# Performance work log

Hardware: AMD Instinct MI355X
Metric: run time of the kernel (lower is better)

## Reference

```python
import jax, jax.numpy as jnp
import numpy as np

N = 100_000   # nodes
E = 1_600_000 # edges
V = 100_000   # vocab
G = 256       # graphs in batch
D = 64        # emb/hidden dim


def setup_inputs() -> dict:
    key = jax.random.key(0)
    ks = jax.random.split(key, 12)
    x_tokens = jax.random.randint(ks[0], (N, 1), 0, V)
    edge_index = jax.random.randint(ks[1], (2, E), 0, N)
    batch = jnp.sort(jax.random.randint(ks[2], (N,), 0, G))
    s = 0.02
    return {
        "x_tokens": x_tokens,
        "edge_index": edge_index,
        "batch": batch,
        "emb_table": jax.random.normal(ks[3], (V, D), jnp.float32) * s,
        "W0": jax.random.normal(ks[4], (D, D), jnp.float32) * s,
        "b0": jnp.zeros((D,), jnp.float32),
        "W1": jax.random.normal(ks[5], (D, D), jnp.float32) * s,
        "b1": jnp.zeros((D,), jnp.float32),
        "W2": jax.random.normal(ks[6], (D, D), jnp.float32) * s,
        "b2": jnp.zeros((D,), jnp.float32),
        "Wc1": jax.random.normal(ks[7], (2 * D, D), jnp.float32) * s,
        "bc1": jnp.zeros((D,), jnp.float32),
        "Wc2": jax.random.normal(ks[8], (D, 2), jnp.float32) * s,
        "bc2": jnp.zeros((2,), jnp.float32),
    }


def _gcn_norm(edge_index, n_nodes):
    # add self loops, compute symmetric normalization coefficients
    loop = jnp.arange(n_nodes, dtype=edge_index.dtype)
    src = jnp.concatenate([edge_index[0], loop])
    dst = jnp.concatenate([edge_index[1], loop])
    deg = jax.ops.segment_sum(jnp.ones_like(dst, jnp.float32), dst, num_segments=n_nodes)
    dinv = jnp.where(deg > 0, deg ** -0.5, 0.0)
    norm = dinv[src] * dinv[dst]  # [E+N]
    return src, dst, norm


def _gcn_conv(x, W, b, src, dst, norm, n_nodes):
    x = x @ W                                   # [N, D]
    msg = x[src] * norm[:, None]                # gather + scale, [E+N, D]
    out = jax.ops.segment_sum(msg, dst, num_segments=n_nodes)
    return out + b


def reference(x_tokens, edge_index, batch, emb_table, W0, b0, W1, b1, W2, b2, Wc1, bc1, Wc2, bc2):
    n = x_tokens.shape[0]
    src, dst, norm = _gcn_norm(edge_index, n)
    x = emb_table[x_tokens[:, 0]]               # [N, D]
    for W, b in ((W0, b0), (W1, b1), (W2, b2)):
        x = jax.nn.relu(_gcn_conv(x, W, b, src, dst, norm, n))
    # dual pooling over graph ids
    cnt = jax.ops.segment_sum(jnp.ones((n,), x.dtype), batch, num_segments=G)
    h_sum = jax.ops.segment_sum(x, batch, num_segments=G)
    h_mean = h_sum / jnp.maximum(cnt, 1.0)[:, None]
    h_max = jax.ops.segment_max(x, batch, num_segments=G)
    h_max = jnp.where(jnp.isfinite(h_max), h_max, 0.0)
    h = jnp.concatenate([h_mean, h_max], axis=-1)   # [G, 2D]
    logits = jax.nn.relu(h @ Wc1 + bc1) @ Wc2 + bc2  # [G, 2]
    return logits
```

## Files before the change

kernel.cpp:

```cpp
#include <hip/hip_runtime.h>
#include <hip/hip_fp16.h>
#include <math.h>


#define BKT_LOG 9
#define BKT (1 << BKT_LOG)
#define CHUNK 4096

typedef _Float16 h2 __attribute__((ext_vector_type(2)));
typedef _Float16 f16x8 __attribute__((ext_vector_type(8)));
typedef float f32x4 __attribute__((ext_vector_type(4)));

__global__ __launch_bounds__(256) void k_wcvt(const float* __restrict__ W0,
                                              const float* __restrict__ W1,
                                              const float* __restrict__ W2,
                                              _Float16* __restrict__ Wf,
                                              int* __restrict__ gcur,
                                              float* __restrict__ hz, int hzn) {
  if (blockIdx.x < 3) {
    const float* W = (blockIdx.x == 0) ? W0 : (blockIdx.x == 1) ? W1 : W2;
    _Float16* out = Wf + blockIdx.x * 4096;
    for (int i = threadIdx.x; i < 4096; i += 256) {
      int c = i >> 10, s = (i >> 9) & 1, l = (i >> 3) & 63, j = i & 7;
      int k = 32 * s + 8 * (l >> 4) + j;
      int ncol = 16 * c + (l & 15);
      out[i] = (_Float16)W[k * 64 + ncol];
    }
  } else if (blockIdx.x == 3) {
    gcur[threadIdx.x] = 0;
  } else {
    for (int i = threadIdx.x; i < hzn; i += 256) hz[i] = 0.f;
  }
}

__global__ __launch_bounds__(256) void k_part(const int* __restrict__ src,
                                              const int* __restrict__ dst,
                                              int* __restrict__ gcur,
                                              int* __restrict__ ebuf,
                                              int E, int S) {
  __shared__ int sA[CHUNK];
  __shared__ int dA[CHUNK];
  __shared__ int h[256], base[256];
  int tid = threadIdx.x;
  long c0 = (long)blockIdx.x * CHUNK;
  int m = (int)min((long)CHUNK, (long)E - c0);
  h[tid] = 0;
  __syncthreads();
  for (int i = tid; i < m; i += 256) {
    int s = src[c0 + i];
    int d = dst[c0 + i];
    sA[i] = s;
    dA[i] = d;
    atomicAdd(&h[d >> BKT_LOG], 1);
  }
  __syncthreads();
  if (h[tid]) base[tid] = atomicAdd(&gcur[tid], h[tid]);
  __syncthreads();
  h[tid] = 0;
  __syncthreads();
  for (int i = tid; i < m; i += 256) {
    int s = sA[i], d = dA[i];
    int k = d >> BKT_LOG;
    int p = base[k] + atomicAdd(&h[k], 1);
    if (p < S)
      ebuf[k * S + p] = ((d & (BKT - 1)) << 17) | s;
  }
}

__global__ __launch_bounds__(512) void k_bplace(const int* __restrict__ ebuf,
                                                const int* __restrict__ gcur,
                                                int* __restrict__ off,
                                                int* __restrict__ eend,
                                                int* __restrict__ csrc,
                                                float* __restrict__ dinv,
                                                int N, int S) {
  __shared__ int s[512];
  __shared__ int cur[512];
  int b = blockIdx.x, tid = threadIdx.x;
  int n0 = b << BKT_LOG;
  int nn = min(BKT, N - n0);
  int e0 = b * S;
  int cnt = min(gcur[b], S);
  s[tid] = 0;
  __syncthreads();
  for (int e = tid; e < cnt; e += 512) atomicAdd(&s[ebuf[e0 + e] >> 17], 1);
  __syncthreads();
  int deg = s[tid];
  for (int d = 1; d < 512; d <<= 1) {
    int t = (tid >= d) ? s[tid - d] : 0;
    __syncthreads();
    s[tid] += t;
    __syncthreads();
  }
  int excl = s[tid] - deg;
  if (tid < nn) {
    off[n0 + tid] = e0 + excl;
    eend[n0 + tid] = e0 + excl + deg;
    dinv[n0 + tid] = 1.0f / sqrtf((float)(1 + deg));
  }
  cur[tid] = excl;
  __syncthreads();
  for (int e = tid; e < cnt; e += 512) {
    int p = ebuf[e0 + e];
    int pos = e0 + atomicAdd(&cur[p >> 17], 1);
    csrc[pos] = p & 0x1FFFF;
  }
}

template <bool EMB>
__global__ __launch_bounds__(256) void k_mfmamm(const _Float16* __restrict__ y,
                                                const int* __restrict__ tok,
                                                const float* __restrict__ emb,
                                                const _Float16* __restrict__ Wf,
                                                const float* __restrict__ dinv,
                                                float scale,
                                                _Float16* __restrict__ xh,
                                                int n) {
  __shared__ _Float16 lds[4 * 16 * 72];
  int w = threadIdx.x >> 6, l = threadIdx.x & 63;
  int m = l & 15, q = l >> 4;
  int rbase = blockIdx.x * 64 + w * 16;

  f16x8 a0, a1;
  if (EMB) {
    int node = min(rbase + m, n - 1);
    const float* er = emb + (size_t)tok[node] * 64;
    float4 v0 = *(const float4*)(er + q * 8);
    float4 v1 = *(const float4*)(er + q * 8 + 4);
    float4 v2 = *(const float4*)(er + 32 + q * 8);
    float4 v3 = *(const float4*)(er + 32 + q * 8 + 4);
    a0[0] = (_Float16)v0.x; a0[1] = (_Float16)v0.y; a0[2] = (_Float16)v0.z; a0[3] = (_Float16)v0.w;
    a0[4] = (_Float16)v1.x; a0[5] = (_Float16)v1.y; a0[6] = (_Float16)v1.z; a0[7] = (_Float16)v1.w;
    a1[0] = (_Float16)v2.x; a1[1] = (_Float16)v2.y; a1[2] = (_Float16)v2.z; a1[3] = (_Float16)v2.w;
    a1[4] = (_Float16)v3.x; a1[5] = (_Float16)v3.y; a1[6] = (_Float16)v3.z; a1[7] = (_Float16)v3.w;
  } else {
    int node = rbase + m;
    const _Float16* yr = y + ((size_t)(unsigned)node << 6);
    a0 = *(const f16x8*)(yr + q * 8);
    a1 = *(const f16x8*)(yr + 32 + q * 8);
  }
  float4 d4 = *(const float4*)(dinv + rbase + q * 4);

  const f16x8* wf = (const f16x8*)Wf + l;
  f32x4 acc[4];
#pragma unroll
  for (int c = 0; c < 4; c++) {
    f32x4 z = {0.f, 0.f, 0.f, 0.f};
    z = __builtin_amdgcn_mfma_f32_16x16x32_f16(a0, wf[(c * 2 + 0) * 64], z, 0, 0, 0);
    z = __builtin_amdgcn_mfma_f32_16x16x32_f16(a1, wf[(c * 2 + 1) * 64], z, 0, 0, 0);
    acc[c] = z;
  }

  const float ds[4] = {d4.x * scale, d4.y * scale, d4.z * scale, d4.w * scale};
  _Float16* ldw = lds + w * 16 * 72;
#pragma unroll
  for (int c = 0; c < 4; c++)
#pragma unroll
    for (int r = 0; r < 4; r++)
      ldw[(q * 4 + r) * 72 + c * 16 + m] = (_Float16)(acc[c][r] * ds[r]);
  __syncthreads();

  int row2 = l & 15, c2 = l >> 4;
  int node = rbase + row2;
  if (node < n) {
    const uint4* s4 = (const uint4*)(ldw + row2 * 72 + c2 * 16);
    uint4 v0 = s4[0], v1 = s4[1];
    uint4* dst = (uint4*)(xh + ((size_t)(unsigned)node << 6) + c2 * 16);
    dst[0] = v0;
    dst[1] = v1;
  }
}

__global__ __launch_bounds__(256) void k_aggregate(const int* __restrict__ off,
                                                   const int* __restrict__ eend,
                                                   const int* __restrict__ csrc,
                                                   const float* __restrict__ dinv,
                                                   const _Float16* __restrict__ xh,
                                                   const float* __restrict__ bias,
                                                   _Float16* __restrict__ outp,
                                                   int n) {
  int lane = threadIdx.x & 63;
  int t = __builtin_amdgcn_readfirstlane(blockIdx.x * 4 + (threadIdx.x >> 6));
  if (t >= n) return;
  int e0 = off[t];
  int e1 = eend[t];

  float acc = (float)xh[((size_t)(unsigned)t << 6) + lane];
  int e = e0;
  for (; e + 4 <= e1; e += 4) {
    int s0 = csrc[e];
    int s1 = csrc[e + 1];
    int s2 = csrc[e + 2];
    int s3 = csrc[e + 3];
    float v0 = (float)xh[((size_t)(unsigned)s0 << 6) + lane];
    float v1 = (float)xh[((size_t)(unsigned)s1 << 6) + lane];
    float v2 = (float)xh[((size_t)(unsigned)s2 << 6) + lane];
    float v3 = (float)xh[((size_t)(unsigned)s3 << 6) + lane];
    acc += v0;
    acc += v1;
    acc += v2;
    acc += v3;
  }
  for (; e < e1; ++e)
    acc += (float)xh[((size_t)(unsigned)csrc[e] << 6) + lane];

  float sc = dinv[t] * (1.0f / 256.0f);
  float o = fmaxf(acc * sc + bias[lane], 0.f) * 4096.f;
  outp[((size_t)(unsigned)t << 6) + lane] = (_Float16)o;
}

__global__ __launch_bounds__(256) void k_pool(const _Float16* __restrict__ x,
                                              const int* __restrict__ batch,
                                              float* __restrict__ hsum,
                                              float* __restrict__ hmax,
                                              int* __restrict__ cntg,
                                              int n) {
  int wid = (blockIdx.x * blockDim.x + threadIdx.x) >> 6;
  int lane = threadIdx.x & 63;
  int i0 = wid * 64;
  if (i0 >= n) return;
  int i1 = min(i0 + 64, n);
  int batch_l = (i0 + lane < n) ? batch[i0 + lane] : 0;
  float gsum = 0.f, gmax = 0.f;
  int cur = __shfl(batch_l, 0);
  int c = 0;
  for (int i = i0; i < i1; i++) {
    int g = __shfl(batch_l, i - i0);
    if (g != cur) {
      atomicAdd(&hsum[cur * 64 + lane], gsum);
      atomicMax((int*)&hmax[cur * 64 + lane], __float_as_int(gmax));
      if (lane == 0) atomicAdd(&cntg[cur], c);
      gsum = 0.f; gmax = 0.f; c = 0; cur = g;
    }
    float v = (float)x[((size_t)(unsigned)i << 6) + lane];
    gsum += v;
    gmax = fmaxf(gmax, v);
    c++;
  }
  atomicAdd(&hsum[cur * 64 + lane], gsum);
  atomicMax((int*)&hmax[cur * 64 + lane], __float_as_int(gmax));
  if (lane == 0) atomicAdd(&cntg[cur], c);
}

__global__ __launch_bounds__(64) void k_cls(const float* __restrict__ hsum,
                                            const float* __restrict__ hmax,
                                            const int* __restrict__ cnt,
                                            const float* __restrict__ Wc1,
                                            const float* __restrict__ bc1,
                                            const float* __restrict__ Wc2,
                                            const float* __restrict__ bc2,
                                            float* __restrict__ out) {
  __shared__ float h[128];
  __shared__ float hid[64];
  int g = blockIdx.x, j = threadIdx.x;
  int c = cnt[g];
  float cf = (float)(c > 0 ? c : 1);
  h[j] = hsum[g * 64 + j] / cf * (1.0f / 4096.0f);
  h[64 + j] = hmax[g * 64 + j] * (1.0f / 4096.0f);
  __syncthreads();
  float acc = bc1[j];
  for (int k = 0; k < 128; k++) acc += h[k] * Wc1[k * 64 + j];
  hid[j] = fmaxf(acc, 0.f);
  __syncthreads();
  if (j < 2) {
    float a = bc2[j];
    for (int k = 0; k < 64; k++) a += hid[k] * Wc2[k * 2 + j];
    out[g * 2 + j] = a;
  }
}

extern "C" void kernel_launch(void* const* d_in, const int* in_sizes, int n_in,
                              void* d_out, int out_size, void* d_ws, size_t ws_size,
                              hipStream_t stream) {
  const int N = in_sizes[0];
  const int E = in_sizes[1] / 2;
  const int G = out_size / 2;
  const int B = (N + BKT - 1) >> BKT_LOG;
  const int Npad = (N + 63) & ~63;
  const int S = ((((E + B - 1) / B) * 3 / 2 + 256) + 3) & ~3;

  const int* tok   = (const int*)d_in[0];
  const int* ei    = (const int*)d_in[1];
  const int* batch = (const int*)d_in[2];
  const float* emb = (const float*)d_in[3];
  const float* W0 = (const float*)d_in[4];  const float* b0 = (const float*)d_in[5];
  const float* W1 = (const float*)d_in[6];  const float* b1 = (const float*)d_in[7];
  const float* W2 = (const float*)d_in[8];  const float* b2 = (const float*)d_in[9];
  const float* Wc1 = (const float*)d_in[10]; const float* bc1 = (const float*)d_in[11];
  const float* Wc2 = (const float*)d_in[12]; const float* bc2 = (const float*)d_in[13];
  const int* srcp = ei;
  const int* dstp = ei + E;

  int* off    = (int*)d_ws;
  int* eend   = off + N;
  float* dinv = (float*)(eend + N);
  int* gcur   = (int*)(dinv + Npad);
  _Float16* Wf = (_Float16*)(gcur + 256);
  int* csrc   = (int*)(Wf + 3 * 4096);
  _Float16* xh = (_Float16*)(csrc + (size_t)B * S);
  _Float16* y  = xh + (size_t)Npad * 64;
  int* ebuf   = (int*)y;
  float* hsum = (float*)(y + (size_t)Npad * 64);
  float* hmax = hsum + (size_t)G * 64;
  int*   cntg = (int*)(hmax + (size_t)G * 64);

  auto cdiv = [](long a, long b) { return (int)((a + b - 1) / b); };
  const int aggBlocks = cdiv(N, 4);

  k_wcvt<<<5, 256, 0, stream>>>(W0, W1, W2, Wf, gcur, hsum, G * 129);

  k_part<<<cdiv(E, CHUNK), 256, 0, stream>>>(srcp, dstp, gcur, ebuf, E, S);
  k_bplace<<<B, 512, 0, stream>>>(ebuf, gcur, off, eend, csrc, dinv, N, S);

  k_mfmamm<true><<<cdiv(N, 64), 256, 0, stream>>>(nullptr, tok, emb, Wf, dinv, 256.f, xh, N);
  k_aggregate<<<aggBlocks, 256, 0, stream>>>(off, eend, csrc, dinv, xh, b0, y, N);

  k_mfmamm<false><<<cdiv(N, 64), 256, 0, stream>>>(y, nullptr, nullptr, Wf + 4096, dinv, 1.f / 16.f, xh, N);
  k_aggregate<<<aggBlocks, 256, 0, stream>>>(off, eend, csrc, dinv, xh, b1, y, N);

  k_mfmamm<false><<<cdiv(N, 64), 256, 0, stream>>>(y, nullptr, nullptr, Wf + 8192, dinv, 1.f / 16.f, xh, N);
  k_aggregate<<<aggBlocks, 256, 0, stream>>>(off, eend, csrc, dinv, xh, b2, y, N);

  k_pool<<<cdiv(N, 256), 256, 0, stream>>>(y, batch, hsum, hmax, cntg, N);

  k_cls<<<G, 64, 0, stream>>>(hsum, hmax, cntg, Wc1, bc1, Wc2, bc2, (float*)d_out);
}
```

Measured before the change: 342.5 us.

## Fold self-loop into CSR and gather 4-half chunks per lane in aggregation

The bucket placement kernel now writes each node's self-loop into its CSR neighbour list and folds it into the degree, so aggregation needs no separate self term. The aggregation kernel is restructured: each wavefront splits into 4 groups of 16 lanes, each group loads 8 neighbour indices as int4 vectors and gathers 8-byte chunks of the feature row. Values are accumulated with fdot2 against unit masks, then reduced across groups with shuffles. This aims to cut per-edge index loads and issue wider gathers with more loads in flight, at the cost of masked tail handling, a shuffle reduction, and only a quarter of lanes storing.

```diff
diff --git a/kernel.cpp b/kernel.cpp
--- a/kernel.cpp
+++ b/kernel.cpp
@@ -8,8 +8,31 @@
 #define CHUNK 4096
 
 typedef _Float16 h2 __attribute__((ext_vector_type(2)));
+typedef _Float16 f16x4 __attribute__((ext_vector_type(4)));
 typedef _Float16 f16x8 __attribute__((ext_vector_type(8)));
 typedef float f32x4 __attribute__((ext_vector_type(4)));
+
+union HU { unsigned u; h2 h; };
+__device__ inline h2 h2bits(unsigned u) { HU x; x.u = u; return x.h; }
+
+#if __has_builtin(__builtin_amdgcn_fdot2)
+#define FDOT2(a, b, c) __builtin_amdgcn_fdot2((a), (b), (c), false)
+#else
+__device__ inline float FDOT2(h2 a, h2 b, float c) {
+  return (float)a.x * (float)b.x + (float)a.y * (float)b.y + c;
+}
+#endif
+
+#define MASK_X 0x00003C00u
+#define MASK_Y 0x3C000000u
+
+__device__ inline void acc4c(uint2 v, float& a0, float& a1, float& a2, float& a3) {
+  h2 lo = h2bits(v.x), hi = h2bits(v.y);
+  a0 = FDOT2(lo, h2bits(MASK_X), a0);
+  a1 = FDOT2(lo, h2bits(MASK_Y), a1);
+  a2 = FDOT2(hi, h2bits(MASK_X), a2);
+  a3 = FDOT2(hi, h2bits(MASK_Y), a3);
+}
 
 __global__ __launch_bounds__(256) void k_wcvt(const float* __restrict__ W0,
                                               const float* __restrict__ W1,
@@ -80,25 +103,26 @@
   int n0 = b << BKT_LOG;
   int nn = min(BKT, N - n0);
   int e0 = b * S;
-  int cnt = min(gcur[b], S);
-  s[tid] = 0;
+  int cnt = min(gcur[b], S - nn);
+  s[tid] = (tid < nn) ? 1 : 0;
   __syncthreads();
   for (int e = tid; e < cnt; e += 512) atomicAdd(&s[ebuf[e0 + e] >> 17], 1);
   __syncthreads();
-  int deg = s[tid];
+  int degws = s[tid];
   for (int d = 1; d < 512; d <<= 1) {
     int t = (tid >= d) ? s[tid - d] : 0;
     __syncthreads();
     s[tid] += t;
     __syncthreads();
   }
-  int excl = s[tid] - deg;
+  int excl = s[tid] - degws;
   if (tid < nn) {
     off[n0 + tid] = e0 + excl;
-    eend[n0 + tid] = e0 + excl + deg;
-    dinv[n0 + tid] = 1.0f / sqrtf((float)(1 + deg));
-  }
-  cur[tid] = excl;
+    eend[n0 + tid] = e0 + excl + degws;
+    dinv[n0 + tid] = 1.0f / sqrtf((float)degws);
+    csrc[e0 + excl] = n0 + tid;
+  }
+  cur[tid] = excl + ((tid < nn) ? 1 : 0);
   __syncthreads();
   for (int e = tid; e < cnt; e += 512) {
     int p = ebuf[e0 + e];
@@ -180,33 +204,55 @@
                                                    _Float16* __restrict__ outp,
                                                    int n) {
   int lane = threadIdx.x & 63;
-  int t = __builtin_amdgcn_readfirstlane(blockIdx.x * 4 + (threadIdx.x >> 6));
+  int t = blockIdx.x * 4 + (threadIdx.x >> 6);
   if (t >= n) return;
   int e0 = off[t];
   int e1 = eend[t];
-
-  float acc = (float)xh[((size_t)(unsigned)t << 6) + lane];
-  int e = e0;
-  for (; e + 4 <= e1; e += 4) {
-    int s0 = csrc[e];
-    int s1 = csrc[e + 1];
-    int s2 = csrc[e + 2];
-    int s3 = csrc[e + 3];
-    float v0 = (float)xh[((size_t)(unsigned)s0 << 6) + lane];
-    float v1 = (float)xh[((size_t)(unsigned)s1 << 6) + lane];
-    float v2 = (float)xh[((size_t)(unsigned)s2 << 6) + lane];
-    float v3 = (float)xh[((size_t)(unsigned)s3 << 6) + lane];
-    acc += v0;
-    acc += v1;
-    acc += v2;
-    acc += v3;
-  }
-  for (; e < e1; ++e)
-    acc += (float)xh[((size_t)(unsigned)csrc[e] << 6) + lane];
-
-  float sc = dinv[t] * (1.0f / 256.0f);
-  float o = fmaxf(acc * sc + bias[lane], 0.f) * 4096.f;
-  outp[((size_t)(unsigned)t << 6) + lane] = (_Float16)o;
+  int p = lane >> 4;
+  int f = lane & 15;
+  const char* xb = (const char*)xh;
+
+  float a0 = 0.f, a1 = 0.f, a2 = 0.f, a3 = 0.f;
+  for (int base = (e0 & ~7); base < e1; base += 32) {
+    int my = base + p * 8;
+    int4 iA = {0, 0, 0, 0}, iB = {0, 0, 0, 0};
+    if (my < e1) iA = *(const int4*)(csrc + my);
+    if (my + 4 < e1) iB = *(const int4*)(csrc + my + 4);
+    uint2 v0 = {0,0}, v1 = {0,0}, v2 = {0,0}, v3 = {0,0};
+    uint2 v4 = {0,0}, v5 = {0,0}, v6 = {0,0}, v7 = {0,0};
+    if (my + 0 >= e0 && my + 0 < e1) v0 = *(const uint2*)(xb + ((size_t)(unsigned)iA.x << 7) + f * 8);
+    if (my + 1 >= e0 && my + 1 < e1) v1 = *(const uint2*)(xb + ((size_t)(unsigned)iA.y << 7) + f * 8);
+    if (my + 2 >= e0 && my + 2 < e1) v2 = *(const uint2*)(xb + ((size_t)(unsigned)iA.z << 7) + f * 8);
+    if (my + 3 >= e0 && my + 3 < e1) v3 = *(const uint2*)(xb + ((size_t)(unsigned)iA.w << 7) + f * 8);
+    if (my + 4 >= e0 && my + 4 < e1) v4 = *(const uint2*)(xb + ((size_t)(unsigned)iB.x << 7) + f * 8);
+    if (my + 5 >= e0 && my + 5 < e1) v5 = *(const uint2*)(xb + ((size_t)(unsigned)iB.y << 7) + f * 8);
+    if (my + 6 >= e0 && my + 6 < e1) v6 = *(const uint2*)(xb + ((size_t)(unsigned)iB.z << 7) + f * 8);
+    if (my + 7 >= e0 && my + 7 < e1) v7 = *(const uint2*)(xb + ((size_t)(unsigned)iB.w << 7) + f * 8);
+    acc4c(v0, a0, a1, a2, a3);
+    acc4c(v1, a0, a1, a2, a3);
+    acc4c(v2, a0, a1, a2, a3);
+    acc4c(v3, a0, a1, a2, a3);
+    acc4c(v4, a0, a1, a2, a3);
+    acc4c(v5, a0, a1, a2, a3);
+    acc4c(v6, a0, a1, a2, a3);
+    acc4c(v7, a0, a1, a2, a3);
+  }
+
+  a0 += __shfl_xor(a0, 16); a0 += __shfl_xor(a0, 32);
+  a1 += __shfl_xor(a1, 16); a1 += __shfl_xor(a1, 32);
+  a2 += __shfl_xor(a2, 16); a2 += __shfl_xor(a2, 32);
+  a3 += __shfl_xor(a3, 16); a3 += __shfl_xor(a3, 32);
+
+  if (p == 0) {
+    float sc = dinv[t] * (1.0f / 256.0f);
+    float4 bb = *(const float4*)(bias + f * 4);
+    f16x4 hv;
+    hv[0] = (_Float16)(fmaxf(a0 * sc + bb.x, 0.f) * 4096.f);
+    hv[1] = (_Float16)(fmaxf(a1 * sc + bb.y, 0.f) * 4096.f);
+    hv[2] = (_Float16)(fmaxf(a2 * sc + bb.z, 0.f) * 4096.f);
+    hv[3] = (_Float16)(fmaxf(a3 * sc + bb.w, 0.f) * 4096.f);
+    *(f16x4*)((char*)outp + ((size_t)(unsigned)t << 7) + f * 8) = hv;
+  }
 }
 
 __global__ __launch_bounds__(256) void k_pool(const _Float16* __restrict__ x,
@@ -277,7 +323,7 @@
   const int G = out_size / 2;
   const int B = (N + BKT - 1) >> BKT_LOG;
   const int Npad = (N + 63) & ~63;
-  const int S = ((((E + B - 1) / B) * 3 / 2 + 256) + 3) & ~3;
+  const int S = ((((E + B - 1) / B) * 3 / 2 + 256) + 7) & ~7;
 
   const int* tok   = (const int*)d_in[0];
   const int* ei    = (const int*)d_in[1];
```

Result: faster. 332.3 us (-3.0%).
